# Optimization experiments

Hardware: AMD Instinct MI355X
Metric: run time of the kernel (lower is better)

## Reference

```python
import jax, jax.numpy as jnp
import numpy as np

K = -1.0          # manifold curvature (hyperbolic / Poincare ball)
SK = 1.0          # sqrt(|K|)
EPS = 1e-7


def _artan_k(x):
    # inverse of tan_k for K<0: artanh(sqrt(|K|) x)/sqrt(|K|)
    return jnp.arctanh(jnp.clip(SK * x, -1.0 + EPS, 1.0 - EPS)) / SK


def _tan_k(x):
    return jnp.tanh(SK * x) / SK


def _norm(x):
    return jnp.maximum(jnp.linalg.norm(x, axis=-1, keepdims=True), 1e-15)


def mobius_add(x, y):
    xy = jnp.sum(x * y, -1, keepdims=True)
    x2 = jnp.sum(x * x, -1, keepdims=True)
    y2 = jnp.sum(y * y, -1, keepdims=True)
    num = (1.0 - 2.0 * K * xy - K * y2) * x + (1.0 + K * x2) * y
    den = 1.0 - 2.0 * K * xy + K * K * x2 * y2
    return num / jnp.maximum(den, 1e-15)


def mobius_scalar_mul(r, x):
    # r may be scalar or (n,1) per-row scalar
    xn = _norm(x)
    return _tan_k(r * _artan_k(xn)) * x / xn


def mobius_matvec(W, x):
    # geoopt convention: (m @ x) per point -> x @ W^T
    xn = _norm(x)
    mx = x @ W.T
    mxn = _norm(mx)
    return _tan_k(mxn / xn * _artan_k(xn)) * mx / mxn


def lambda_x(x):
    # conformal factor lambda_x = 2 / (1 + K |x|^2); returns shape (...,)
    return 2.0 / jnp.maximum(1.0 + K * jnp.sum(x * x, -1), 1e-10)


def expmap0(u):
    un = _norm(u)
    return _tan_k(un) * u / un


def logmap0(y):
    yn = _norm(y)
    return _artan_k(yn) * y / yn


def kappa_left_multiply(A, X):
    # Vectorized per-node weighted gyro-midpoint + mobius scalar mul.
    # out_i = (sum_j A_ij) otimes gyromidpoint(X, weights=A_i)
    gamma = lambda_x(X)                              # (n,)
    denom = A @ (gamma - 1.0)                        # (n,)
    denom = jnp.where(jnp.abs(denom) < 1e-10, 1e-10, denom)
    nom = A @ (gamma[:, None] * X)                   # (n,d)
    two_mean = nom / denom[:, None]
    m = mobius_scalar_mul(0.5, two_mean)             # gyromidpoint
    return mobius_scalar_mul(jnp.sum(A, axis=1, keepdims=True), m)


def setup_inputs() -> dict:
    key = jax.random.key(0)
    k1, k2, k3, k4, k5 = jax.random.split(key, 5)
    n, d, c = 8192, 256, 16
    # node embeddings on the Poincare ball (small norm, well inside the ball)
    X = 0.01 * jax.random.normal(k1, (n, d), jnp.float32)
    # dense normalized adjacency (positive weights, row sums O(1))
    A_hat = jax.random.uniform(k2, (n, n), dtype=jnp.float32) / n
    W = jax.random.uniform(k3, (d, d), dtype=jnp.float32)        # torch.rand init
    W_logits = jax.random.uniform(k4, (d, c), dtype=jnp.float32)
    # p_ks = expmap0(rand), scaled for numerical stability
    p_ks = expmap0(0.05 * jax.random.uniform(k5, (c, d), dtype=jnp.float32))
    return {"X": X, "A_hat": A_hat, "W": W, "W_logits": W_logits, "p_ks": p_ks}


def reference(X, A_hat, W, W_logits, p_ks):
    # hidden kappa-GCN layer
    XW = mobius_matvec(W, X)                          # (n,d)
    AXW = kappa_left_multiply(A_hat, XW)              # (n,d)
    H1 = expmap0(jax.nn.relu(logmap0(AXW)))           # manifold.apply(relu)
    # hyperbolic logits (kappa != 0 branch, K<0 -> asinh)
    z = mobius_add(-p_ks[None, :, :], H1[:, None, :]) # (n,k,d)
    z_n = jnp.linalg.norm(z, axis=-1)                 # (n,k)
    a_n = jnp.maximum(jnp.linalg.norm(W_logits, axis=0), 1e-15)  # (k,)
    za = jnp.einsum('nkd,dk->nk', z, W_logits)
    den = jnp.maximum(1.0 + K * z_n * z_n, 1e-10) * a_n
    dist = jnp.arcsinh(2.0 * SK * za / den)
    lam = lambda_x(p_ks)                              # (k,)
    logits = (lam * a_n / SK) * dist                  # (n,k)
    return A_hat @ logits
```

## Files before the change

### kernel.cpp

```cpp
#include <hip/hip_runtime.h>
#include <math.h>

#define Nn 8192
#define Dd 256
#define Cc 16

#define OFF_BP   4194304u
#define OFF_LOG  5242880u
#define OFF_G1B  5373952u
#define OFF_DEN  5378048u
#define OFF_RS   5410816u
#define OFF_KC   5443584u
#define WS_FLOATS 5443648u

typedef short vshort8 __attribute__((ext_vector_type(8)));
typedef float vfloat4 __attribute__((ext_vector_type(4)));

#define AS1 __attribute__((address_space(1)))
#define AS3 __attribute__((address_space(3)))

__device__ __forceinline__ float clip1(float x) {
    return fminf(fmaxf(x, -1.0f + 1e-7f), 1.0f - 1e-7f);
}

__device__ __forceinline__ unsigned short f2bf(float f) {
    unsigned int u = __float_as_uint(f);
    u += 0x7fff + ((u >> 16) & 1);
    return (unsigned short)(u >> 16);
}

__device__ __forceinline__ float bf2f(unsigned short b) {
    return __uint_as_float(((unsigned int)b) << 16);
}

__device__ __forceinline__ float waveReduce(float v) {
    #pragma unroll
    for (int off = 32; off; off >>= 1) v += __shfl_down(v, off);
    return v;
}

__device__ __forceinline__ float blockReduceBcast(float v, float* red) {
    int t = threadIdx.x, w = t >> 6, l = t & 63;
    v = waveReduce(v);
    if (l == 0) red[w] = v;
    __syncthreads();
    if (t == 0) red[0] = red[0] + red[1] + red[2] + red[3];
    __syncthreads();
    float r = red[0];
    __syncthreads();
    return r;
}

__global__ __launch_bounds__(256) void k_consts(const float* __restrict__ Wl,
                                                const float* __restrict__ Pk,
                                                float* __restrict__ kc) {
    __shared__ float red[8];
    int t = threadIdx.x, k = blockIdx.x;
    float pv = Pk[k * Dd + t];
    float wv = Wl[t * Cc + k];
    float p2 = blockReduceBcast(pv * pv, red);
    float pw = blockReduceBcast(pv * wv, red);
    float w2 = blockReduceBcast(wv * wv, red);
    if (t == 0) {
        float an  = fmaxf(sqrtf(w2), 1e-15f);
        float lam = 2.0f / fmaxf(1.0f - p2, 1e-10f);
        kc[k * 4 + 0] = p2; kc[k * 4 + 1] = pw;
        kc[k * 4 + 2] = an; kc[k * 4 + 3] = lam;
    }
}

__global__ __launch_bounds__(256) void k_front(const float* __restrict__ X,
                                               const float* __restrict__ W,
                                               unsigned short* __restrict__ Bp,
                                               unsigned short* __restrict__ g1b) {
    __shared__ __align__(16) unsigned short Xs[32][256];
    __shared__ __align__(16) unsigned short Gs[32][258];
    __shared__ float xs2[32];
    __shared__ float scal[32];
    __shared__ float red4[32][4];

    const int t = threadIdx.x;
    const int l = t & 63, w = t >> 6;
    const int ll = l & 15, kh = l >> 4;
    const int m0 = blockIdx.x * 32;
    const int ar = t >> 3, aq = t & 7;
    const int c0 = w * 64;

    float x2p = 0.f;
    #pragma unroll
    for (int tc = 0; tc < 4; ++tc) {
        const float* xp = &X[(size_t)(m0 + ar) * Dd + tc * 64 + aq * 8];
        vfloat4 v0 = *(const vfloat4*)xp;
        vfloat4 v1 = *(const vfloat4*)(xp + 4);
        vshort8 o;
        #pragma unroll
        for (int e = 0; e < 4; ++e) {
            x2p += v0[e] * v0[e] + v1[e] * v1[e];
            o[e] = (short)f2bf(v0[e]);
            o[e + 4] = (short)f2bf(v1[e]);
        }
        int byte = (tc * 64 + aq * 8) * 2;
        *(vshort8*)((char*)&Xs[ar][0] + (byte ^ ((ar & 7) << 4))) = o;
    }
    x2p += __shfl_xor(x2p, 1); x2p += __shfl_xor(x2p, 2); x2p += __shfl_xor(x2p, 4);
    if (aq == 0) xs2[ar] = x2p;
    __syncthreads();

    vfloat4 acc[2][4];
    #pragma unroll
    for (int mi = 0; mi < 2; ++mi)
        #pragma unroll
        for (int ni = 0; ni < 4; ++ni)
            acc[mi][ni] = (vfloat4){0.f, 0.f, 0.f, 0.f};
    #pragma unroll
    for (int tc = 0; tc < 4; ++tc) {
        vshort8 bf[8];
        #pragma unroll
        for (int ni = 0; ni < 4; ++ni)
            #pragma unroll
            for (int kk = 0; kk < 2; ++kk) {
                const float* wp = &W[(size_t)(c0 + ni * 16 + ll) * Dd
                                     + tc * 64 + kh * 8 + kk * 32];
                vfloat4 b0 = *(const vfloat4*)wp;
                vfloat4 b1 = *(const vfloat4*)(wp + 4);
                vshort8 o;
                #pragma unroll
                for (int e = 0; e < 4; ++e) {
                    o[e] = (short)f2bf(b0[e]);
                    o[e + 4] = (short)f2bf(b1[e]);
                }
                bf[ni * 2 + kk] = o;
            }
        #pragma unroll
        for (int kk = 0; kk < 2; ++kk) {
            int byte = (tc * 64 + kh * 8 + kk * 32) * 2;
            vshort8 af[2];
            #pragma unroll
            for (int mi = 0; mi < 2; ++mi) {
                int row = mi * 16 + ll;
                af[mi] = *(const vshort8*)((const char*)&Xs[row][0]
                                           + (byte ^ ((row & 7) << 4)));
            }
            #pragma unroll
            for (int mi = 0; mi < 2; ++mi)
                #pragma unroll
                for (int ni = 0; ni < 4; ++ni)
                    acc[mi][ni] = __builtin_amdgcn_mfma_f32_16x16x32_bf16(
                        af[mi], bf[ni * 2 + kk], acc[mi][ni], 0, 0, 0);
        }
    }

    #pragma unroll
    for (int mi = 0; mi < 2; ++mi)
        #pragma unroll
        for (int j = 0; j < 4; ++j) {
            float p = 0.f;
            #pragma unroll
            for (int ni = 0; ni < 4; ++ni)
                p += acc[mi][ni][j] * acc[mi][ni][j];
            p += __shfl_xor(p, 1); p += __shfl_xor(p, 2);
            p += __shfl_xor(p, 4); p += __shfl_xor(p, 8);
            if (ll == 0) red4[mi * 16 + kh * 4 + j][w] = p;
        }
    __syncthreads();

    if (t < 32) {
        float mx2 = red4[t][0] + red4[t][1] + red4[t][2] + red4[t][3];
        float xn = fmaxf(sqrtf(xs2[t]), 1e-15f);
        float mxn = fmaxf(sqrtf(mx2), 1e-15f);
        float s = tanhf(mxn / xn * atanhf(clip1(xn))) / mxn;
        float xw2 = s * s * mx2;
        float gamma = 2.0f / fmaxf(1.0f - xw2, 1e-10f);
        scal[t] = gamma * s;
        g1b[m0 + t] = f2bf(gamma - 1.0f);
    }
    __syncthreads();

    #pragma unroll
    for (int mi = 0; mi < 2; ++mi)
        #pragma unroll
        for (int ni = 0; ni < 4; ++ni) {
            int row = mi * 16 + kh * 4;
            int col = c0 + ni * 16 + ll;
            #pragma unroll
            for (int j = 0; j < 4; ++j)
                Gs[row + j][col] = f2bf(scal[row + j] * acc[mi][ni][j]);
        }
    __syncthreads();

    const int s = blockIdx.x;
    #pragma unroll
    for (int pass = 0; pass < 4; ++pass) {
        int c = pass * 256 + t;
        int gni = c >> 6, lc = c & 63;
        int col = (gni >> 2) * 64 + (gni & 3) * 16 + (lc & 15);
        int kh8 = (lc >> 4) * 8;
        vshort8 o;
        #pragma unroll
        for (int e = 0; e < 8; ++e) o[e] = (short)Gs[kh8 + e][col];
        *(vshort8*)&Bp[((size_t)(s * 16 + gni) * 64 + lc) * 8] = o;
    }
}

__device__ __forceinline__ void g1_issueB(const unsigned short* __restrict__ Bp,
        unsigned short (&Bs)[2][16][512], int bbuf, int splt, int slab,
        int w, int l) {
    #pragma unroll
    for (int ni = 0; ni < 4; ++ni)
        __builtin_amdgcn_global_load_lds(
            (const AS1 unsigned int*)
                (Bp + ((size_t)((splt * 64 + slab) * 16 + w * 4 + ni) * 512) + l * 8),
            (AS3 unsigned int*)&Bs[bbuf][w * 4 + ni][0], 16, 0, 0);
}

__device__ __forceinline__ void g1_issueA(const float* const (&asrc)[2],
        float (&As)[4][2048], int buf, int w, int tile) {
    #pragma unroll
    for (int i = 0; i < 2; ++i)
        __builtin_amdgcn_global_load_lds(
            (const AS1 unsigned int*)(asrc[i] + tile * 32),
            (AS3 unsigned int*)&As[buf][i * 1024 + w * 256], 16, 0, 0);
}

__device__ __forceinline__ void g1_phase(const float (&As)[4][2048],
        const unsigned short (&Bs)[2][16][512], const unsigned short* g1s,
        int cur, int bbuf, int p, int w, int kh, int ll15, int l,
        vfloat4 (&acc)[4][4], float (&dacc)[4], float (&racc)[4]) {
    vshort8 gv = {};
    if (w == 0) gv = *(const vshort8*)&g1s[p * 32 + kh * 8];
    vshort8 bf[4];
    #pragma unroll
    for (int ni = 0; ni < 4; ++ni)
        bf[ni] = *(const vshort8*)&Bs[bbuf][w * 4 + ni][l * 8];
    vshort8 af[4];
    #pragma unroll
    for (int mi = 0; mi < 4; ++mi) {
        int row = mi * 16 + ll15;
        int ba = row * 128 + (((kh * 2) ^ (row & 7)) << 4);
        vfloat4 v0 = *(const vfloat4*)((const char*)&As[cur][0] + ba);
        vfloat4 v1 = *(const vfloat4*)((const char*)&As[cur][0] + (ba ^ 16));
        vshort8 o;
        #pragma unroll
        for (int e = 0; e < 4; ++e) {
            o[e] = (short)f2bf(v0[e]);
            o[e + 4] = (short)f2bf(v1[e]);
        }
        af[mi] = o;
        if (w == 0) {
            #pragma unroll
            for (int e = 0; e < 4; ++e) {
                dacc[mi] += v0[e] * bf2f((unsigned short)gv[e])
                          + v1[e] * bf2f((unsigned short)gv[e + 4]);
                racc[mi] += v0[e] + v1[e];
            }
        }
    }
    #pragma unroll
    for (int mi = 0; mi < 4; ++mi)
        #pragma unroll
        for (int ni = 0; ni < 4; ++ni)
            acc[mi][ni] = __builtin_amdgcn_mfma_f32_16x16x32_bf16(
                af[mi], bf[ni], acc[mi][ni], 0, 0, 0);
}

__global__ __launch_bounds__(256, 2) void k_gemm1_mfma(
        const float* __restrict__ A,
        const unsigned short* __restrict__ Bp,
        const unsigned short* __restrict__ g1b,
        unsigned short* __restrict__ Pp,
        float* __restrict__ denp,
        float* __restrict__ rsp) {
    __shared__ __align__(16) float As[4][2048];
    __shared__ __align__(16) unsigned short Bs[2][16][512];
    __shared__ __align__(16) unsigned short g1s[2048];

    const int t = threadIdx.x, l = t & 63, w = t >> 6;
    const int id = blockIdx.x;
    const int splt = id & 3;
    const int m0 = (id >> 2) * 64;
    const int kb = splt * 2048;
    const int kh = l >> 4, ll15 = l & 15;

    const float* asrc[2];
    #pragma unroll
    for (int i = 0; i < 2; ++i) {
        int q = i * 256 + t;
        int row = q >> 3, c = q & 7;
        asrc[i] = &A[(size_t)(m0 + row) * Nn + kb + ((c ^ (row & 7)) << 2)];
    }

    vfloat4 acc[4][4];
    #pragma unroll
    for (int mi = 0; mi < 4; ++mi)
        #pragma unroll
        for (int ni = 0; ni < 4; ++ni)
            acc[mi][ni] = (vfloat4){0.f, 0.f, 0.f, 0.f};
    float dacc[4] = {0.f, 0.f, 0.f, 0.f}, racc[4] = {0.f, 0.f, 0.f, 0.f};

    {
        uint4 g1v = *(const uint4*)&g1b[kb + t * 8];
        *(uint4*)&g1s[t * 8] = g1v;
        g1_issueB(Bp, Bs, 0, splt, 0, w, l);
        g1_issueA(asrc, As, 0, w, 0);
        g1_issueA(asrc, As, 1, w, 1);
        g1_issueA(asrc, As, 2, w, 2);
        asm volatile("s_waitcnt vmcnt(4) lgkmcnt(0)" ::: "memory");
        __builtin_amdgcn_s_barrier();
        __builtin_amdgcn_sched_barrier(0);
    }

    for (int u = 0; u < 15; ++u) {
        #pragma unroll
        for (int pp = 0; pp < 4; ++pp) {
            const int p = u * 4 + pp;
            g1_issueB(Bp, Bs, (pp & 1) ^ 1, splt, p + 1, w, l);
            g1_issueA(asrc, As, (pp + 3) & 3, w, p + 3);
            asm volatile("s_waitcnt vmcnt(8)" ::: "memory");
            g1_phase(As, Bs, g1s, pp, pp & 1, p, w, kh, ll15, l, acc, dacc, racc);
            __builtin_amdgcn_s_barrier();
            __builtin_amdgcn_sched_barrier(0);
        }
    }
    g1_issueB(Bp, Bs, 1, splt, 61, w, l);
    g1_issueA(asrc, As, 3, w, 63);
    asm volatile("s_waitcnt vmcnt(8)" ::: "memory");
    g1_phase(As, Bs, g1s, 0, 0, 60, w, kh, ll15, l, acc, dacc, racc);
    __builtin_amdgcn_s_barrier();
    __builtin_amdgcn_sched_barrier(0);

    g1_issueB(Bp, Bs, 0, splt, 62, w, l);
    asm volatile("s_waitcnt vmcnt(6)" ::: "memory");
    g1_phase(As, Bs, g1s, 1, 1, 61, w, kh, ll15, l, acc, dacc, racc);
    __builtin_amdgcn_s_barrier();
    __builtin_amdgcn_sched_barrier(0);

    g1_issueB(Bp, Bs, 1, splt, 63, w, l);
    asm volatile("s_waitcnt vmcnt(4)" ::: "memory");
    g1_phase(As, Bs, g1s, 2, 0, 62, w, kh, ll15, l, acc, dacc, racc);
    __builtin_amdgcn_s_barrier();
    __builtin_amdgcn_sched_barrier(0);

    asm volatile("s_waitcnt vmcnt(0)" ::: "memory");
    g1_phase(As, Bs, g1s, 3, 1, 63, w, kh, ll15, l, acc, dacc, racc);

    if (w == 0) {
        #pragma unroll
        for (int mi = 0; mi < 4; ++mi) {
            dacc[mi] += __shfl_xor(dacc[mi], 16);
            dacc[mi] += __shfl_xor(dacc[mi], 32);
            racc[mi] += __shfl_xor(racc[mi], 16);
            racc[mi] += __shfl_xor(racc[mi], 32);
        }
        if (l < 16) {
            #pragma unroll
            for (int mi = 0; mi < 4; ++mi) {
                denp[splt * Nn + m0 + mi * 16 + l] = dacc[mi];
                rsp [splt * Nn + m0 + mi * 16 + l] = racc[mi];
            }
        }
    }

    unsigned short* P = Pp + (size_t)splt * ((size_t)Nn * Dd);
    #pragma unroll
    for (int mi = 0; mi < 4; ++mi)
        #pragma unroll
        for (int ni = 0; ni < 4; ++ni) {
            int row = m0 + mi * 16 + (kh << 2);
            int col = w * 64 + ni * 16 + ll15;
            #pragma unroll
            for (int j = 0; j < 4; ++j)
                P[(size_t)(row + j) * Dd + col] = f2bf(acc[mi][ni][j]);
        }
}

__global__ __launch_bounds__(256) void k_rowfix(const unsigned short* __restrict__ Pp,
                                                const float* __restrict__ denp,
                                                const float* __restrict__ rsp,
                                                const float* __restrict__ Pk,
                                                const float* __restrict__ Wl,
                                                const float* __restrict__ kc,
                                                float* __restrict__ logits) {
    __shared__ float red[8];
    __shared__ float hs[256];
    __shared__ float PQ[16][2];
    int i = blockIdx.x, t = threadIdx.x;
    float nom = 0.f;
    #pragma unroll
    for (int s = 0; s < 4; ++s)
        nom += bf2f(Pp[(size_t)s * Nn * Dd + (size_t)i * Dd + t]);
    float dv = denp[i] + denp[Nn + i] + denp[2 * Nn + i] + denp[3 * Nn + i];
    dv = (fabsf(dv) < 1e-10f) ? 1e-10f : dv;
    float tm = nom / dv;
    float r2 = blockReduceBcast(tm * tm, red);
    float r = fmaxf(sqrtf(r2), 1e-15f);
    float mmul = tanhf(0.5f * atanhf(clip1(r))) / r;
    float mj = mmul * tm;
    float mn2 = blockReduceBcast(mj * mj, red);
    float mn = fmaxf(sqrtf(mn2), 1e-15f);
    float sA = rsp[i] + rsp[Nn + i] + rsp[2 * Nn + i] + rsp[3 * Nn + i];
    float axmul = tanhf(sA * atanhf(clip1(mn))) / mn;
    float axw = axmul * mj;
    float yn2 = blockReduceBcast(axw * axw, red);
    float yn = fmaxf(sqrtf(yn2), 1e-15f);
    float v = atanhf(clip1(yn)) / yn * axw;
    float u = fmaxf(v, 0.0f);
    float un2 = blockReduceBcast(u * u, red);
    float un = fmaxf(sqrtf(un2), 1e-15f);
    float h = tanhf(un) / un * u;
    float h2 = blockReduceBcast(h * h, red);
    hs[t] = h;
    __syncthreads();
    int w = t >> 6, l = t & 63;
    #pragma unroll
    for (int kk = 0; kk < 4; ++kk) {
        int k = w * 4 + kk;
        float pp = 0.f, qq = 0.f;
        #pragma unroll
        for (int m = 0; m < 4; ++m) {
            float hv = hs[l + 64 * m];
            pp += hv * Pk[k * Dd + l + 64 * m];
            qq += hv * Wl[(l + 64 * m) * Cc + k];
        }
        pp = waveReduce(pp);
        qq = waveReduce(qq);
        if (l == 0) { PQ[k][0] = pp; PQ[k][1] = qq; }
    }
    __syncthreads();
    if (t < 16) {
        int k = t;
        float p2 = kc[k * 4 + 0], pw = kc[k * 4 + 1];
        float an = kc[k * 4 + 2], lam = kc[k * 4 + 3];
        float P = PQ[k][0], Q = PQ[k][1];
        float alpha = 1.0f - 2.0f * P + h2;
        float beta  = 1.0f - p2;
        float Dm = fmaxf(1.0f - 2.0f * P + p2 * h2, 1e-15f);
        float za  = (-alpha * pw + beta * Q) / Dm;
        float zn2 = (alpha * alpha * p2 - 2.0f * alpha * beta * P + beta * beta * h2)
                    / (Dm * Dm);
        float dd = fmaxf(1.0f - zn2, 1e-10f) * an;
        float dist = asinhf(2.0f * za / dd);
        logits[(size_t)i * Cc + k] = lam * an * dist;
    }
}

__global__ __launch_bounds__(256) void k_gemm2(const float* __restrict__ A,
                                               const float* __restrict__ L,
                                               float* __restrict__ part) {
    __shared__ __align__(16) float Ls[64 * 20];
    __shared__ float Pacc[256 * 16];
    int t = threadIdx.x;
    int r0 = blockIdx.x * 256;
    int jbase = blockIdx.y * 512;
    int q = t & 3, g = t >> 2;
    float acc[4][16] = {};
    for (int jc = 0; jc < 512; jc += 64) {
        {
            int jrow = t >> 2, kq = t & 3;
            *(float4*)&Ls[jrow * 20 + kq * 4] =
                *(const float4*)&L[(size_t)(jbase + jc + jrow) * Cc + kq * 4];
        }
        __syncthreads();
        #pragma unroll
        for (int m = 0; m < 4; ++m) {
            int jl = m * 16 + q * 4;
            float av[4][4];
            #pragma unroll
            for (int rr = 0; rr < 4; ++rr) {
                float4 tmp = *(const float4*)&A[(size_t)(r0 + g * 4 + rr) * Nn
                                                + jbase + jc + jl];
                av[rr][0] = tmp.x; av[rr][1] = tmp.y;
                av[rr][2] = tmp.z; av[rr][3] = tmp.w;
            }
            #pragma unroll
            for (int jj = 0; jj < 4; ++jj) {
                const float* lr = &Ls[(jl + jj) * 20];
                float lv[16];
                #pragma unroll
                for (int k2 = 0; k2 < 16; k2 += 4) {
                    float4 lt = *(const float4*)&lr[k2];
                    lv[k2] = lt.x; lv[k2 + 1] = lt.y;
                    lv[k2 + 2] = lt.z; lv[k2 + 3] = lt.w;
                }
                #pragma unroll
                for (int rr = 0; rr < 4; ++rr)
                    #pragma unroll
                    for (int k2 = 0; k2 < 16; ++k2)
                        acc[rr][k2] += av[rr][jj] * lv[k2];
            }
        }
        __syncthreads();
    }
    for (int ii = t; ii < 4096; ii += 256) Pacc[ii] = 0.f;
    __syncthreads();
    for (int qq = 0; qq < 4; ++qq) {
        if (q == qq) {
            #pragma unroll
            for (int rr = 0; rr < 4; ++rr)
                #pragma unroll
                for (int k2 = 0; k2 < 16; ++k2)
                    Pacc[(g * 4 + rr) * 16 + k2] += acc[rr][k2];
        }
        __syncthreads();
    }
    float* dst = &part[(size_t)blockIdx.y * (Nn * Cc) + (size_t)r0 * Cc];
    for (int ii = t * 4; ii < 4096; ii += 1024)
        *(float4*)&dst[ii] = *(const float4*)&Pacc[ii];
}

__global__ __launch_bounds__(256) void k_reduce(const float* __restrict__ part,
                                                float* __restrict__ out) {
    int i = blockIdx.x * 256 + threadIdx.x;
    float s = 0.f;
    #pragma unroll
    for (int j = 0; j < 16; ++j) s += part[(size_t)j * (Nn * Cc) + i];
    out[i] = s;
}

extern "C" void kernel_launch(void* const* d_in, const int* in_sizes, int n_in,
                              void* d_out, int out_size, void* d_ws, size_t ws_size,
                              hipStream_t stream) {
    const float* X  = (const float*)d_in[0];
    const float* A  = (const float*)d_in[1];
    const float* W  = (const float*)d_in[2];
    const float* Wl = (const float*)d_in[3];
    const float* Pk = (const float*)d_in[4];
    float* out = (float*)d_out;
    float* ws = (float*)d_ws;
    if (ws_size < (size_t)WS_FLOATS * sizeof(float)) return;

    unsigned short* Pp  = (unsigned short*)ws;
    float* part = ws;
    unsigned short* Bp  = (unsigned short*)(ws + OFF_BP);
    float* lg   = ws + OFF_LOG;
    unsigned short* g1b = (unsigned short*)(ws + OFF_G1B);
    float* denp = ws + OFF_DEN;
    float* rsp  = ws + OFF_RS;
    float* kc   = ws + OFF_KC;

    k_consts<<<16, 256, 0, stream>>>(Wl, Pk, kc);
    k_front<<<256, 256, 0, stream>>>(X, W, Bp, g1b);
    k_gemm1_mfma<<<512, 256, 0, stream>>>(A, Bp, g1b, Pp, denp, rsp);
    k_rowfix<<<Nn, 256, 0, stream>>>(Pp, denp, rsp, Pk, Wl, kc, lg);
    k_gemm2<<<dim3(32, 16), 256, 0, stream>>>(A, lg, part);
    k_reduce<<<512, 256, 0, stream>>>(part, out);
}
```

Before: 235.9 us.

## Convert A tile to bf16 once in registers before staging to LDS in gemm1

The A tile is no longer loaded as fp32 into a 4-deep LDS ring via direct global-to-LDS copies. Each thread now loads 8 fp32 values into registers, converts them to bf16, accumulates the gamma-weighted denominator and row sum, and writes a swizzled bf16 tile into a double-buffered LDS. Before, each wave converted the same A fragments redundantly and wave 0 alone did the reductions. Conversion and reduction work is now spread across all threads and LDS footprint drops, at the cost of register-staged loads with a shallower prefetch depth and extra LDS writes.

After: 220.4 us. 6.6% less time.

```diff
diff --git a/kernel.cpp b/kernel.cpp
--- a/kernel.cpp
+++ b/kernel.cpp
@@ -202,58 +202,50 @@
     }
 }
 
-__device__ __forceinline__ void g1_issueB(const unsigned short* __restrict__ Bp,
-        unsigned short (&Bs)[2][16][512], int bbuf, int splt, int slab,
-        int w, int l) {
+__device__ __forceinline__ void g2_issueB(const unsigned short* __restrict__ Bp,
+        unsigned short (&BsB)[16][512], int splt, int slab, int w, int l) {
     #pragma unroll
     for (int ni = 0; ni < 4; ++ni)
         __builtin_amdgcn_global_load_lds(
             (const AS1 unsigned int*)
                 (Bp + ((size_t)((splt * 64 + slab) * 16 + w * 4 + ni) * 512) + l * 8),
-            (AS3 unsigned int*)&Bs[bbuf][w * 4 + ni][0], 16, 0, 0);
-}
-
-__device__ __forceinline__ void g1_issueA(const float* const (&asrc)[2],
-        float (&As)[4][2048], int buf, int w, int tile) {
-    #pragma unroll
-    for (int i = 0; i < 2; ++i)
-        __builtin_amdgcn_global_load_lds(
-            (const AS1 unsigned int*)(asrc[i] + tile * 32),
-            (AS3 unsigned int*)&As[buf][i * 1024 + w * 256], 16, 0, 0);
-}
-
-__device__ __forceinline__ void g1_phase(const float (&As)[4][2048],
-        const unsigned short (&Bs)[2][16][512], const unsigned short* g1s,
-        int cur, int bbuf, int p, int w, int kh, int ll15, int l,
-        vfloat4 (&acc)[4][4], float (&dacc)[4], float (&racc)[4]) {
-    vshort8 gv = {};
-    if (w == 0) gv = *(const vshort8*)&g1s[p * 32 + kh * 8];
-    vshort8 bf[4];
+            (AS3 unsigned int*)&BsB[w * 4 + ni][0], 16, 0, 0);
+}
+
+__device__ __forceinline__ void g2_loadA(const float* __restrict__ Abase,
+                                         int tile, float (&a8)[8]) {
+    const vfloat4* p = (const vfloat4*)(Abase + tile * 32);
+    *(vfloat4*)&a8[0] = p[0];
+    *(vfloat4*)&a8[4] = p[1];
+}
+
+__device__ __forceinline__ void g2_stage(unsigned short (&AsB)[2048],
+        const unsigned short* g1s, const float (&a8)[8],
+        int tile, int rowst, int kq, float& dacc, float& racc) {
+    vshort8 gv = *(const vshort8*)&g1s[tile * 32 + kq * 8];
+    vshort8 o;
+    #pragma unroll
+    for (int e = 0; e < 8; ++e) {
+        float av = a8[e];
+        o[e] = (short)f2bf(av);
+        dacc += av * bf2f((unsigned short)gv[e]);
+        racc += av;
+    }
+    *(vshort8*)((char*)&AsB[0] + rowst * 64 + ((kq * 16) ^ ((rowst & 3) << 4))) = o;
+}
+
+__device__ __forceinline__ void g2_mfma(const unsigned short (&AsB)[2048],
+        const unsigned short (&BsB)[16][512], int w, int kh, int ll15, int l,
+        vfloat4 (&acc)[4][4]) {
+    vshort8 bf[4], af[4];
     #pragma unroll
     for (int ni = 0; ni < 4; ++ni)
-        bf[ni] = *(const vshort8*)&Bs[bbuf][w * 4 + ni][l * 8];
-    vshort8 af[4];
+        bf[ni] = *(const vshort8*)&BsB[w * 4 + ni][l * 8];
     #pragma unroll
     for (int mi = 0; mi < 4; ++mi) {
         int row = mi * 16 + ll15;
-        int ba = row * 128 + (((kh * 2) ^ (row & 7)) << 4);
-        vfloat4 v0 = *(const vfloat4*)((const char*)&As[cur][0] + ba);
-        vfloat4 v1 = *(const vfloat4*)((const char*)&As[cur][0] + (ba ^ 16));
-        vshort8 o;
-        #pragma unroll
-        for (int e = 0; e < 4; ++e) {
-            o[e] = (short)f2bf(v0[e]);
-            o[e + 4] = (short)f2bf(v1[e]);
-        }
-        af[mi] = o;
-        if (w == 0) {
-            #pragma unroll
-            for (int e = 0; e < 4; ++e) {
-                dacc[mi] += v0[e] * bf2f((unsigned short)gv[e])
-                          + v1[e] * bf2f((unsigned short)gv[e + 4]);
-                racc[mi] += v0[e] + v1[e];
-            }
-        }
+        af[mi] = *(const vshort8*)((const char*)&AsB[0]
+                  + row * 64 + ((kh * 16) ^ ((row & 3) << 4)));
     }
     #pragma unroll
     for (int mi = 0; mi < 4; ++mi)
@@ -270,7 +262,7 @@
         unsigned short* __restrict__ Pp,
         float* __restrict__ denp,
         float* __restrict__ rsp) {
-    __shared__ __align__(16) float As[4][2048];
+    __shared__ __align__(16) unsigned short As[2][2048];
     __shared__ __align__(16) unsigned short Bs[2][16][512];
     __shared__ __align__(16) unsigned short g1s[2048];
 
@@ -280,14 +272,9 @@
     const int m0 = (id >> 2) * 64;
     const int kb = splt * 2048;
     const int kh = l >> 4, ll15 = l & 15;
-
-    const float* asrc[2];
-    #pragma unroll
-    for (int i = 0; i < 2; ++i) {
-        int q = i * 256 + t;
-        int row = q >> 3, c = q & 7;
-        asrc[i] = &A[(size_t)(m0 + row) * Nn + kb + ((c ^ (row & 7)) << 2)];
-    }
+    const int rowst = t >> 2, kq = t & 3;
+
+    const float* Abase = &A[(size_t)(m0 + rowst) * Nn + kb + kq * 8];
 
     vfloat4 acc[4][4];
     #pragma unroll
@@ -295,69 +282,58 @@
         #pragma unroll
         for (int ni = 0; ni < 4; ++ni)
             acc[mi][ni] = (vfloat4){0.f, 0.f, 0.f, 0.f};
-    float dacc[4] = {0.f, 0.f, 0.f, 0.f}, racc[4] = {0.f, 0.f, 0.f, 0.f};
+    float dacc = 0.f, racc = 0.f;
+    float a0[8], a1[8];
 
     {
         uint4 g1v = *(const uint4*)&g1b[kb + t * 8];
         *(uint4*)&g1s[t * 8] = g1v;
-        g1_issueB(Bp, Bs, 0, splt, 0, w, l);
-        g1_issueA(asrc, As, 0, w, 0);
-        g1_issueA(asrc, As, 1, w, 1);
-        g1_issueA(asrc, As, 2, w, 2);
-        asm volatile("s_waitcnt vmcnt(4) lgkmcnt(0)" ::: "memory");
+    }
+    g2_issueB(Bp, Bs[0], splt, 0, w, l);
+    g2_loadA(Abase, 0, a0);
+    g2_loadA(Abase, 1, a1);
+    asm volatile("s_waitcnt lgkmcnt(0)" ::: "memory");
+    __builtin_amdgcn_s_barrier();
+    asm volatile("s_waitcnt vmcnt(2)" ::: "memory");
+    g2_stage(As[0], g1s, a0, 0, rowst, kq, dacc, racc);
+    asm volatile("s_waitcnt lgkmcnt(0)" ::: "memory");
+    __builtin_amdgcn_s_barrier();
+    __builtin_amdgcn_sched_barrier(0);
+
+    for (int u = 0; u < 31; ++u) {
+        const int p = u * 2;
+        g2_issueB(Bp, Bs[1], splt, p + 1, w, l);
+        g2_loadA(Abase, p + 2, a0);
+        asm volatile("s_waitcnt vmcnt(6)" ::: "memory");
+        g2_stage(As[1], g1s, a1, p + 1, rowst, kq, dacc, racc);
+        g2_mfma(As[0], Bs[0], w, kh, ll15, l, acc);
+        asm volatile("s_waitcnt lgkmcnt(0)" ::: "memory");
         __builtin_amdgcn_s_barrier();
         __builtin_amdgcn_sched_barrier(0);
-    }
-
-    for (int u = 0; u < 15; ++u) {
-        #pragma unroll
-        for (int pp = 0; pp < 4; ++pp) {
-            const int p = u * 4 + pp;
-            g1_issueB(Bp, Bs, (pp & 1) ^ 1, splt, p + 1, w, l);
-            g1_issueA(asrc, As, (pp + 3) & 3, w, p + 3);
-            asm volatile("s_waitcnt vmcnt(8)" ::: "memory");
-            g1_phase(As, Bs, g1s, pp, pp & 1, p, w, kh, ll15, l, acc, dacc, racc);
-            __builtin_amdgcn_s_barrier();
-            __builtin_amdgcn_sched_barrier(0);
-        }
-    }
-    g1_issueB(Bp, Bs, 1, splt, 61, w, l);
-    g1_issueA(asrc, As, 3, w, 63);
-    asm volatile("s_waitcnt vmcnt(8)" ::: "memory");
-    g1_phase(As, Bs, g1s, 0, 0, 60, w, kh, ll15, l, acc, dacc, racc);
+        g2_issueB(Bp, Bs[0], splt, p + 2, w, l);
+        g2_loadA(Abase, p + 3, a1);
+        asm volatile("s_waitcnt vmcnt(6)" ::: "memory");
+        g2_stage(As[0], g1s, a0, p + 2, rowst, kq, dacc, racc);
+        g2_mfma(As[1], Bs[1], w, kh, ll15, l, acc);
+        asm volatile("s_waitcnt lgkmcnt(0)" ::: "memory");
+        __builtin_amdgcn_s_barrier();
+        __builtin_amdgcn_sched_barrier(0);
+    }
+    g2_issueB(Bp, Bs[1], splt, 63, w, l);
+    asm volatile("s_waitcnt vmcnt(4)" ::: "memory");
+    g2_stage(As[1], g1s, a1, 63, rowst, kq, dacc, racc);
+    g2_mfma(As[0], Bs[0], w, kh, ll15, l, acc);
+    asm volatile("s_waitcnt lgkmcnt(0)" ::: "memory");
     __builtin_amdgcn_s_barrier();
     __builtin_amdgcn_sched_barrier(0);
-
-    g1_issueB(Bp, Bs, 0, splt, 62, w, l);
-    asm volatile("s_waitcnt vmcnt(6)" ::: "memory");
-    g1_phase(As, Bs, g1s, 1, 1, 61, w, kh, ll15, l, acc, dacc, racc);
-    __builtin_amdgcn_s_barrier();
-    __builtin_amdgcn_sched_barrier(0);
-
-    g1_issueB(Bp, Bs, 1, splt, 63, w, l);
-    asm volatile("s_waitcnt vmcnt(4)" ::: "memory");
-    g1_phase(As, Bs, g1s, 2, 0, 62, w, kh, ll15, l, acc, dacc, racc);
-    __builtin_amdgcn_s_barrier();
-    __builtin_amdgcn_sched_barrier(0);
-
     asm volatile("s_waitcnt vmcnt(0)" ::: "memory");
-    g1_phase(As, Bs, g1s, 3, 1, 63, w, kh, ll15, l, acc, dacc, racc);
-
-    if (w == 0) {
-        #pragma unroll
-        for (int mi = 0; mi < 4; ++mi) {
-            dacc[mi] += __shfl_xor(dacc[mi], 16);
-            dacc[mi] += __shfl_xor(dacc[mi], 32);
-            racc[mi] += __shfl_xor(racc[mi], 16);
-            racc[mi] += __shfl_xor(racc[mi], 32);
-        }
-        if (l < 16) {
-            #pragma unroll
-            for (int mi = 0; mi < 4; ++mi) {
-                denp[splt * Nn + m0 + mi * 16 + l] = dacc[mi];
-                rsp [splt * Nn + m0 + mi * 16 + l] = racc[mi];
-            }
-        }
+    g2_mfma(As[1], Bs[1], w, kh, ll15, l, acc);
+
+    dacc += __shfl_xor(dacc, 1); dacc += __shfl_xor(dacc, 2);
+    racc += __shfl_xor(racc, 1); racc += __shfl_xor(racc, 2);
+    if (kq == 0) {
+        denp[splt * Nn + m0 + rowst] = dacc;
+        rsp [splt * Nn + m0 + rowst] = racc;
     }
 
     unsigned short* P = Pp + (size_t)splt * ((size_t)Nn * Dd);
@@ -455,9 +431,9 @@
     float acc[4][16] = {};
     for (int jc = 0; jc < 512; jc += 64) {
         {
-            int jrow = t >> 2, kq = t & 3;
-            *(float4*)&Ls[jrow * 20 + kq * 4] =
-                *(const float4*)&L[(size_t)(jbase + jc + jrow) * Cc + kq * 4];
+            int jrow = t >> 2, kq2 = t & 3;
+            *(float4*)&Ls[jrow * 20 + kq2 * 4] =
+                *(const float4*)&L[(size_t)(jbase + jc + jrow) * Cc + kq2 * 4];
         }
         __syncthreads();
         #pragma unroll
```
